# Kernel tuning notes

Hardware: AMD Instinct MI355X
Metric: run time of the kernel (lower is better)

Reference implementation:

```python
import jax, jax.numpy as jnp
import numpy as np

B, L, D = 2, 2048, 1024
H, NL = 16, 8
DH = D // H  # 64


def setup_inputs() -> dict:
    key = jax.random.key(0)
    ks = jax.random.split(key, 16)
    s_d = 1.0 / np.sqrt(D)
    s_ff = 1.0 / np.sqrt(4 * D)
    f32 = jnp.float32
    return {
        "x": jax.random.normal(ks[0], (B, L, D), f32),
        "pe": jax.random.normal(ks[1], (L, D), f32) / 10.0,
        "wq": jax.random.normal(ks[2], (NL, D, D), f32) * s_d,
        "wk": jax.random.normal(ks[3], (NL, D, D), f32) * s_d,
        "wv": jax.random.normal(ks[4], (NL, D, D), f32) * s_d,
        "ln1_g": 1.0 + 0.02 * jax.random.normal(ks[5], (NL, D), f32),
        "ln1_b": 0.02 * jax.random.normal(ks[6], (NL, D), f32),
        "w1": jax.random.normal(ks[7], (NL, D, 4 * D), f32) * s_d,
        "b1": jax.random.normal(ks[8], (NL, 4 * D), f32) * s_d,
        "w2": jax.random.normal(ks[9], (NL, 4 * D, D), f32) * s_ff,
        "b2": jax.random.normal(ks[10], (NL, D), f32) * s_ff,
        "ln2_g": 1.0 + 0.02 * jax.random.normal(ks[11], (NL, D), f32),
        "ln2_b": 0.02 * jax.random.normal(ks[12], (NL, D), f32),
    }


def _layernorm(x, g, b, eps=1e-5):
    m = jnp.mean(x, axis=-1, keepdims=True)
    v = jnp.mean(jnp.square(x - m), axis=-1, keepdims=True)
    return (x - m) * jax.lax.rsqrt(v + eps) * g + b


def reference(x, pe, wq, wk, wv, ln1_g, ln1_b, w1, b1, w2, b2, ln2_g, ln2_b):
    Bb, T, Dd = x.shape
    h = x + pe[:T]
    causal = jnp.tril(jnp.ones((T, T), dtype=bool))  # [T,T]
    inv_sqrt_dh = np.float32(1.0 / np.sqrt(DH))

    def step(h, p):
        wq_, wk_, wv_, g1, be1, w1_, bb1, w2_, bb2, g2, be2 = p
        # QKV: [B,T,D] -> [B,H,T,DH]
        q = (h @ wq_).reshape(Bb, T, H, DH).transpose(0, 2, 1, 3)
        k = (h @ wk_).reshape(Bb, T, H, DH).transpose(0, 2, 1, 3)
        v = (h @ wv_).reshape(Bb, T, H, DH).transpose(0, 2, 1, 3)
        scores = jnp.einsum('bhqd,bhkd->bhqk', q, k)
        scores = jnp.where(causal, scores, -jnp.inf)
        attn = jax.nn.softmax(scores * inv_sqrt_dh, axis=-1)
        o = jnp.einsum('bhqk,bhkd->bhqd', attn, v)
        o = o.transpose(0, 2, 1, 3).reshape(Bb, T, Dd)
        h = _layernorm(h + o, g1, be1)
        mlp = jax.nn.selu(h @ w1_ + bb1) @ w2_ + bb2
        h = _layernorm(h + mlp, g2, be2)
        return h, None

    h, _ = jax.lax.scan(step, h, (wq, wk, wv, ln1_g, ln1_b, w1, b1, w2, b2, ln2_g, ln2_b))
    return h
```

## Files before the change

kernel.cpp:

```cpp
#include <hip/hip_runtime.h>
#include <stdint.h>

typedef unsigned short u16;
typedef __bf16 bf16x8 __attribute__((ext_vector_type(8)));
typedef __bf16 bf16x4 __attribute__((ext_vector_type(4)));
typedef float f32x4 __attribute__((ext_vector_type(4)));

__device__ __forceinline__ float b2f(u16 b) {
    return __builtin_bit_cast(float, ((unsigned)b) << 16);
}
__device__ __forceinline__ u16 f2b(float f) {
    unsigned u = __builtin_bit_cast(unsigned, f);
    return (u16)((u + 0x7fffu + ((u >> 16) & 1u)) >> 16);
}
__device__ __forceinline__ void async16(const void* g, void* l) {
    __builtin_amdgcn_global_load_lds((const __attribute__((address_space(1))) void*)g,
                                     (__attribute__((address_space(3))) void*)l, 16, 0, 0);
}

__global__ __launch_bounds__(256) void add_pe_kernel(const float* __restrict__ x,
                                                     const float* __restrict__ pe,
                                                     float* __restrict__ hf,
                                                     u16* __restrict__ hb) {
    const size_t i = ((size_t)blockIdx.x * 256 + threadIdx.x) * 4;
    float4 xv = *(const float4*)(x + i);
    float4 pv = *(const float4*)(pe + (i & 2097151));
    float4 f;
    f.x = xv.x + pv.x; f.y = xv.y + pv.y; f.z = xv.z + pv.z; f.w = xv.w + pv.w;
    *(float4*)(hf + i) = f;
    ushort4 hv;
    hv.x = f2b(f.x); hv.y = f2b(f.y); hv.z = f2b(f.z); hv.w = f2b(f.w);
    *(ushort4*)(hb + i) = hv;
}

__global__ __launch_bounds__(256) void transpose_cast_kernel(const float* __restrict__ src0,
                                                             u16* __restrict__ dst0,
                                                             int srcStride, int K,
                                                             int srcLayer, int dstLayer) {
    __shared__ __align__(16) u16 tile[64 * 72];
    const float* src = src0 + (size_t)blockIdx.z * srcLayer;
    u16* dst = dst0 + (size_t)blockIdx.z * dstLayer;
    const int n0 = blockIdx.x * 64, k0 = blockIdx.y * 64;
    const int t = threadIdx.x;
    const int r = t >> 3, c8 = (t & 7) * 8;
#pragma unroll
    for (int ph = 0; ph < 2; ph++) {
        const int rr = r + ph * 32;
        const float* s = src + (size_t)(k0 + rr) * srcStride + n0 + c8;
        float4 a = *(const float4*)s;
        float4 b = *(const float4*)(s + 4);
        u16* tr = tile + rr * 72 + c8;
        tr[0] = f2b(a.x); tr[1] = f2b(a.y); tr[2] = f2b(a.z); tr[3] = f2b(a.w);
        tr[4] = f2b(b.x); tr[5] = f2b(b.y); tr[6] = f2b(b.z); tr[7] = f2b(b.w);
    }
    __syncthreads();
#pragma unroll
    for (int ph = 0; ph < 2; ph++) {
        const int rr = r + ph * 32;
        union { float4 f; u16 u[8]; } ov;
#pragma unroll
        for (int j = 0; j < 8; j++) ov.u[j] = tile[(c8 + j) * 72 + rr];
        *(float4*)(dst + (size_t)(n0 + rr) * K + k0 + c8) = ov.f;
    }
}

__global__ __launch_bounds__(256) void transpose_qkv_kernel(const float* __restrict__ wq,
                                                            const float* __restrict__ wk,
                                                            const float* __restrict__ wv,
                                                            u16* __restrict__ dst) {
    __shared__ __align__(16) u16 tile[64 * 72];
    const int zz = blockIdx.z;
    const int l = zz / 3, mat = zz - l * 3;
    const float* src = ((mat == 0) ? wq : (mat == 1) ? wk : wv) + (size_t)l * 1048576;
    u16* d = dst + (size_t)l * 3145728 + (size_t)mat * 1048576;
    const int n0 = blockIdx.x * 64, k0 = blockIdx.y * 64;
    const int t = threadIdx.x;
    const int r = t >> 3, c8 = (t & 7) * 8;
#pragma unroll
    for (int ph = 0; ph < 2; ph++) {
        const int rr = r + ph * 32;
        const float* s = src + (size_t)(k0 + rr) * 1024 + n0 + c8;
        float4 a = *(const float4*)s;
        float4 b = *(const float4*)(s + 4);
        u16* tr = tile + rr * 72 + c8;
        tr[0] = f2b(a.x); tr[1] = f2b(a.y); tr[2] = f2b(a.z); tr[3] = f2b(a.w);
        tr[4] = f2b(b.x); tr[5] = f2b(b.y); tr[6] = f2b(b.z); tr[7] = f2b(b.w);
    }
    __syncthreads();
#pragma unroll
    for (int ph = 0; ph < 2; ph++) {
        const int rr = r + ph * 32;
        union { float4 f; u16 u[8]; } ov;
#pragma unroll
        for (int j = 0; j < 8; j++) ov.u[j] = tile[(c8 + j) * 72 + rr];
        *(float4*)(d + (size_t)(n0 + rr) * 1024 + k0 + c8) = ov.f;
    }
}

__global__ __launch_bounds__(256) void transpose_v_kernel(const u16* __restrict__ src,
                                                          u16* __restrict__ dst) {
    __shared__ __align__(16) u16 tile[64 * 72];
    const int bh = blockIdx.y, t0 = blockIdx.x * 64;
    const int t = threadIdx.x;
    const int r = t >> 3, c8 = (t & 7) * 8;
    const size_t base = (size_t)bh * 131072;
#pragma unroll
    for (int ph = 0; ph < 2; ph++) {
        const int rr = r + ph * 32;
        *(float4*)(tile + rr * 72 + c8) = *(const float4*)(src + base + (size_t)(t0 + rr) * 64 + c8);
    }
    __syncthreads();
#pragma unroll
    for (int ph = 0; ph < 2; ph++) {
        const int rr = r + ph * 32;
        union { float4 f; u16 u[8]; } ov;
#pragma unroll
        for (int j = 0; j < 8; j++) ov.u[j] = tile[(c8 + j) * 72 + rr];
        *(float4*)(dst + base + (size_t)rr * 2048 + t0 + c8) = ov.f;
    }
}

#define G_SYNC1()                                          \
    __builtin_amdgcn_sched_barrier(0);                     \
    __builtin_amdgcn_s_barrier();                          \
    asm volatile("s_waitcnt lgkmcnt(0)" ::: "memory");     \
    __builtin_amdgcn_sched_barrier(0);                     \
    __builtin_amdgcn_s_setprio(1)
#define G_SYNC2()                                          \
    __builtin_amdgcn_s_setprio(0);                         \
    __builtin_amdgcn_sched_barrier(0);                     \
    __builtin_amdgcn_s_barrier()

template <int MODE, int NT>
__global__ __launch_bounds__(512) void gemm256_kernel(const u16* __restrict__ A,
                                                      const u16* __restrict__ BT,
                                                      const float* __restrict__ bias,
                                                      void* __restrict__ O0, void* __restrict__ O1,
                                                      void* __restrict__ O2, int N, int Kstride) {
    __shared__ __align__(16) u16 lds[65536];
    const int tid = threadIdx.x;
    const int lane = tid & 63, w = tid >> 6, quad = lane >> 4, l15 = lane & 15;
    const int wm = w >> 2, wn = w & 3;
    const int m0 = blockIdx.y * 256, n0 = blockIdx.x * 256;
    const size_t koff = (size_t)blockIdx.z * (NT * 64);

    f32x4 acc[8][4] = {};

    const int srow = tid >> 2;
    const int slog = (tid & 3) ^ ((tid >> 3) & 3);
    const u16* pA = A + (size_t)(m0 + srow) * Kstride + koff + slog * 8;
    const u16* pB = BT + (size_t)(n0 + srow) * Kstride + koff + slog * 8;
    u16* const ldst = lds + tid * 8;

    const int swz = (quad ^ ((l15 >> 1) & 3)) * 8;
    const int aro = (wm * 128 + l15) * 32 + swz;
    const int bro = 16384 + (wn * 64 + l15) * 32 + swz;

    auto stA = [&](int tt, int kh) {
        u16* d = ldst + ((tt & 1) << 15) + (kh << 13);
        const u16* s = pA + tt * 64 + kh * 32;
        async16(s, d);
        async16(s + (size_t)128 * Kstride, d + 4096);
    };
    auto stB = [&](int tt, int kh) {
        u16* d = ldst + ((tt & 1) << 15) + 16384 + (kh << 13);
        const u16* s = pB + tt * 64 + kh * 32;
        async16(s, d);
        async16(s + (size_t)128 * Kstride, d + 4096);
    };

    stB(0, 0); stB(0, 1); stA(0, 0); stA(0, 1);
    stB(1, 0); stB(1, 1); stA(1, 0);
    asm volatile("s_waitcnt vmcnt(6)" ::: "memory");
    __builtin_amdgcn_s_barrier();

#pragma unroll 2
    for (int t = 0; t < NT; ++t) {
        const int boff = (t & 1) << 15;
        bf16x8 a[4], bk0[4], bk1[4];
#pragma unroll
        for (int i = 0; i < 4; i++) a[i] = *(const bf16x8*)(lds + boff + aro + i * 512);
#pragma unroll
        for (int i = 0; i < 4; i++) bk0[i] = *(const bf16x8*)(lds + boff + bro + i * 512);
        if (t + 1 < NT) stA(t + 1, 1);
        G_SYNC1();
#pragma unroll
        for (int mt = 0; mt < 4; mt++)
#pragma unroll
            for (int nt = 0; nt < 4; nt++)
                acc[mt][nt] = __builtin_amdgcn_mfma_f32_16x16x32_bf16(a[mt], bk0[nt], acc[mt][nt], 0, 0, 0);
        G_SYNC2();
#pragma unroll
        for (int i = 0; i < 4; i++) a[i] = *(const bf16x8*)(lds + boff + 8192 + aro + i * 512);
#pragma unroll
        for (int i = 0; i < 4; i++) bk1[i] = *(const bf16x8*)(lds + boff + 8192 + bro + i * 512);
        if (t + 2 < NT) stB(t + 2, 0);
        G_SYNC1();
#pragma unroll
        for (int mt = 0; mt < 4; mt++)
#pragma unroll
            for (int nt = 0; nt < 4; nt++)
                acc[mt][nt] = __builtin_amdgcn_mfma_f32_16x16x32_bf16(a[mt], bk1[nt], acc[mt][nt], 0, 0, 0);
        G_SYNC2();
#pragma unroll
        for (int i = 0; i < 4; i++) a[i] = *(const bf16x8*)(lds + boff + aro + 2048 + i * 512);
        if (t + 2 < NT) stB(t + 2, 1);
        G_SYNC1();
#pragma unroll
        for (int mt = 0; mt < 4; mt++)
#pragma unroll
            for (int nt = 0; nt < 4; nt++)
                acc[4 + mt][nt] = __builtin_amdgcn_mfma_f32_16x16x32_bf16(a[mt], bk0[nt], acc[4 + mt][nt], 0, 0, 0);
        G_SYNC2();
#pragma unroll
        for (int i = 0; i < 4; i++) a[i] = *(const bf16x8*)(lds + boff + 8192 + aro + 2048 + i * 512);
        if (t + 2 < NT) stA(t + 2, 0);
        G_SYNC1();
#pragma unroll
        for (int mt = 0; mt < 4; mt++)
#pragma unroll
            for (int nt = 0; nt < 4; nt++)
                acc[4 + mt][nt] = __builtin_amdgcn_mfma_f32_16x16x32_bf16(a[mt], bk1[nt], acc[4 + mt][nt], 0, 0, 0);
        __builtin_amdgcn_s_setprio(0);
        __builtin_amdgcn_sched_barrier(0);
        if (t < NT - 2) {
            asm volatile("s_waitcnt vmcnt(6)" ::: "memory");
        } else if (t == NT - 2) {
            asm volatile("s_waitcnt vmcnt(0)" ::: "memory");
        }
        __builtin_amdgcn_sched_barrier(0);
        __builtin_amdgcn_s_barrier();
    }

#pragma unroll
    for (int nt = 0; nt < 4; nt++) {
        const int col = n0 + wn * 64 + nt * 16 + l15;
        float bv = 0.f;
        if (MODE == 1) bv = bias[col];
#pragma unroll
        for (int am = 0; am < 8; am++) {
#pragma unroll
            for (int r = 0; r < 4; r++) {
                const int row = m0 + wm * 128 + am * 16 + quad * 4 + r;
                float val = acc[am][nt][r];
                if (MODE == 0) {
                    const int mat = col >> 10, cc = col & 1023;
                    const int head = cc >> 6, dh = cc & 63;
                    const int b = row >> 11, tt = row & 2047;
                    if (mat == 0) val *= 0.18033688f;
                    u16* dst = (mat == 0) ? (u16*)O0 : (mat == 1) ? (u16*)O1 : (u16*)O2;
                    dst[(((size_t)(b * 16 + head)) * 2048 + tt) * 64 + dh] = f2b(val);
                } else if (MODE == 1) {
                    val += bv;
                    const float s = 1.0507009873554805f, aa = 1.6732632423543772f;
                    val = val > 0.f ? s * val : s * aa * (__expf(val) - 1.f);
                    ((u16*)O0)[(size_t)row * N + col] = f2b(val);
                } else if (MODE == 4) {
                    ((float*)O0)[((size_t)blockIdx.z * 4096 + row) * N + col] = val;
                }
            }
        }
    }
}

__global__ __launch_bounds__(256) void attn_kernel(const u16* __restrict__ q,
                                                   const u16* __restrict__ k,
                                                   const u16* __restrict__ vT,
                                                   u16* __restrict__ o) {
    __shared__ __align__(16) u16 Kt[2][4096];
    __shared__ __align__(16) u16 Vt[2][4096];
    __shared__ __align__(16) u16 Pt[4][32 * 72];
    const int tid = threadIdx.x, lane = tid & 63, w = tid >> 6, quad = lane >> 4, l15 = lane & 15;
    const int bh = blockIdx.x;
    const int qt = 15 - blockIdx.y;
    const size_t base = (size_t)bh * 131072;
    const int wrow0 = qt * 128 + w * 32;

    const int r0 = tid >> 3, s0 = (tid & 7) ^ (r0 & 7);
    const int r1 = (tid + 256) >> 3, s1 = (tid & 7) ^ (r1 & 7);
    const u16* kg0 = k + base + r0 * 64 + s0 * 8;
    const u16* kg1 = k + base + r1 * 64 + s1 * 8;
    const u16* vg0 = vT + base + (size_t)r0 * 2048 + s0 * 8;
    const u16* vg1 = vT + base + (size_t)r1 * 2048 + s1 * 8;

    auto stage = [&](int kt, int b) {
        async16(kg0 + kt * 4096, &Kt[b][tid * 8]);
        async16(kg1 + kt * 4096, &Kt[b][tid * 8 + 2048]);
        async16(vg0 + (size_t)kt * 64, &Vt[b][tid * 8]);
        async16(vg1 + (size_t)kt * 64, &Vt[b][tid * 8 + 2048]);
    };

    const int sA = (quad ^ (l15 & 7)) * 8;
    const int sB = sA ^ 32;

    bf16x8 qf[2][2];
#pragma unroll
    for (int nt = 0; nt < 2; nt++)
#pragma unroll
        for (int ks = 0; ks < 2; ks++)
            qf[nt][ks] = *(const bf16x8*)(q + base + (size_t)(wrow0 + nt * 16 + l15) * 64 + ks * 32 + quad * 8);

    float m_[2], l_[2];
    m_[0] = m_[1] = -1e30f;
    l_[0] = l_[1] = 0.f;
    f32x4 oacc[2][4] = {};

    const int ktmax = (qt + 1) * 2;
    stage(0, 0);

    for (int kt = 0; kt < ktmax; kt++) {
        const int cur = kt & 1;
        if (kt + 1 < ktmax) {
            stage(kt + 1, cur ^ 1);
            __builtin_amdgcn_sched_barrier(0);
            asm volatile("s_waitcnt vmcnt(4)" ::: "memory");
        } else {
            __builtin_amdgcn_sched_barrier(0);
            asm volatile("s_waitcnt vmcnt(0)" ::: "memory");
        }
        __builtin_amdgcn_sched_barrier(0);
        __builtin_amdgcn_s_barrier();
        __builtin_amdgcn_sched_barrier(0);
        const u16* Kb = Kt[cur];
        const u16* Vb = Vt[cur];
        const bool act = (kt * 64 <= wrow0 + 31);
        if (act) {
            f32x4 st[4][2];
            __builtin_amdgcn_s_setprio(1);
#pragma unroll
            for (int mt = 0; mt < 4; mt++) {
                bf16x8 kf0 = *(const bf16x8*)(Kb + (mt * 16 + l15) * 64 + sA);
                bf16x8 kf1 = *(const bf16x8*)(Kb + (mt * 16 + l15) * 64 + sB);
#pragma unroll
                for (int nt = 0; nt < 2; nt++) {
                    f32x4 z = {};
                    z = __builtin_amdgcn_mfma_f32_16x16x32_bf16(kf0, qf[nt][0], z, 0, 0, 0);
                    z = __builtin_amdgcn_mfma_f32_16x16x32_bf16(kf1, qf[nt][1], z, 0, 0, 0);
                    st[mt][nt] = z;
                }
            }
            __builtin_amdgcn_s_setprio(0);
            const bool needmask = (kt * 64 + 63 > wrow0);
            float alpha[2];
#pragma unroll
            for (int nt = 0; nt < 2; nt++) {
                const int qg = wrow0 + nt * 16 + l15;
                float mx = -1e30f;
                if (needmask) {
#pragma unroll
                    for (int mt = 0; mt < 4; mt++)
#pragma unroll
                        for (int r = 0; r < 4; r++) {
                            const int kg = kt * 64 + mt * 16 + quad * 4 + r;
                            float s = (kg <= qg) ? st[mt][nt][r] : -1e30f;
                            st[mt][nt][r] = s;
                            mx = fmaxf(mx, s);
                        }
                } else {
#pragma unroll
                    for (int mt = 0; mt < 4; mt++)
#pragma unroll
                        for (int r = 0; r < 4; r++) mx = fmaxf(mx, st[mt][nt][r]);
                }
                mx = fmaxf(mx, __shfl_xor(mx, 16, 64));
                mx = fmaxf(mx, __shfl_xor(mx, 32, 64));
                const float mnew = fmaxf(m_[nt], mx);
                alpha[nt] = exp2f(m_[nt] - mnew);
                m_[nt] = mnew;
                float rs = 0.f;
#pragma unroll
                for (int mt = 0; mt < 4; mt++) {
                    float p0 = exp2f(st[mt][nt][0] - mnew);
                    float p1 = exp2f(st[mt][nt][1] - mnew);
                    float p2 = exp2f(st[mt][nt][2] - mnew);
                    float p3 = exp2f(st[mt][nt][3] - mnew);
                    rs += (p0 + p1) + (p2 + p3);
                    bf16x4 pk = {(__bf16)p0, (__bf16)p1, (__bf16)p2, (__bf16)p3};
                    *(bf16x4*)(Pt[w] + (nt * 16 + l15) * 72 + mt * 16 + quad * 4) = pk;
                }
                rs += __shfl_xor(rs, 16, 64);
                rs += __shfl_xor(rs, 32, 64);
                l_[nt] = l_[nt] * alpha[nt] + rs;
            }
            float arow[2][4];
#pragma unroll
            for (int mto = 0; mto < 2; mto++)
#pragma unroll
                for (int r = 0; r < 4; r++)
                    arow[mto][r] = __shfl(alpha[mto], quad * 4 + r, 64);
#pragma unroll
            for (int mto = 0; mto < 2; mto++)
#pragma unroll
                for (int ntv = 0; ntv < 4; ntv++)
#pragma unroll
                    for (int r = 0; r < 4; r++) oacc[mto][ntv][r] *= arow[mto][r];

            bf16x8 pf[2][2];
#pragma unroll
            for (int mto = 0; mto < 2; mto++)
#pragma unroll
                for (int ks = 0; ks < 2; ks++)
                    pf[mto][ks] = *(const bf16x8*)(Pt[w] + (mto * 16 + l15) * 72 + ks * 32 + quad * 8);
            __builtin_amdgcn_s_setprio(1);
#pragma unroll
            for (int ntv = 0; ntv < 4; ntv++) {
                bf16x8 vf0 = *(const bf16x8*)(Vb + (ntv * 16 + l15) * 64 + sA);
                bf16x8 vf1 = *(const bf16x8*)(Vb + (ntv * 16 + l15) * 64 + sB);
#pragma unroll
                for (int mto = 0; mto < 2; mto++) {
                    oacc[mto][ntv] = __builtin_amdgcn_mfma_f32_16x16x32_bf16(pf[mto][0], vf0, oacc[mto][ntv], 0, 0, 0);
                    oacc[mto][ntv] = __builtin_amdgcn_mfma_f32_16x16x32_bf16(pf[mto][1], vf1, oacc[mto][ntv], 0, 0, 0);
                }
            }
            __builtin_amdgcn_s_setprio(0);
        }
        __builtin_amdgcn_sched_barrier(0);
        __builtin_amdgcn_s_barrier();
        __builtin_amdgcn_sched_barrier(0);
    }

    float linv[2] = {1.f / l_[0], 1.f / l_[1]};
    float rinv[2][4];
#pragma unroll
    for (int mto = 0; mto < 2; mto++)
#pragma unroll
        for (int r = 0; r < 4; r++)
            rinv[mto][r] = __shfl(linv[mto], quad * 4 + r, 64);

    const int b = bh >> 4, hh = bh & 15;
#pragma unroll
    for (int mto = 0; mto < 2; mto++)
#pragma unroll
        for (int ntv = 0; ntv < 4; ntv++)
#pragma unroll
            for (int r = 0; r < 4; r++) {
                const int trow = wrow0 + mto * 16 + quad * 4 + r;
                const int col = hh * 64 + ntv * 16 + l15;
                o[((size_t)b * 2048 + trow) * 1024 + col] = f2b(oacc[mto][ntv][r] * rinv[mto][r]);
            }
}

template <int AM>
__global__ __launch_bounds__(256) void ln_kernel(const float* __restrict__ hin,
                                                 const void* __restrict__ addp,
                                                 const float* __restrict__ g,
                                                 const float* __restrict__ bt,
                                                 const float* __restrict__ bias2,
                                                 float* __restrict__ hf_out,
                                                 u16* __restrict__ hb_out) {
    const int w = threadIdx.x >> 6, lane = threadIdx.x & 63;
    const size_t row = (size_t)blockIdx.x * 4 + w;
    const float4* hr = (const float4*)(hin + row * 1024);
    float4 xv[4];
    float s = 0.f, s2 = 0.f;
#pragma unroll
    for (int j = 0; j < 4; j++) {
        const int idx = lane + 64 * j;
        float4 a = hr[idx];
        float4 b;
        if (AM == 1) {
            ushort4 av = ((const ushort4*)addp)[row * 256 + idx];
            b.x = b2f(av.x); b.y = b2f(av.y); b.z = b2f(av.z); b.w = b2f(av.w);
        } else {
            const float4* pp = (const float4*)addp;
            const size_t po = row * 256 + idx;
            float4 p0 = pp[po];
            float4 p1 = pp[po + 1048576];
            float4 p2 = pp[po + 2097152];
            float4 p3 = pp[po + 3145728];
            float4 bb2 = ((const float4*)bias2)[idx];
            b.x = (p0.x + p1.x) + (p2.x + p3.x) + bb2.x;
            b.y = (p0.y + p1.y) + (p2.y + p3.y) + bb2.y;
            b.z = (p0.z + p1.z) + (p2.z + p3.z) + bb2.z;
            b.w = (p0.w + p1.w) + (p2.w + p3.w) + bb2.w;
        }
        float4 x;
        x.x = a.x + b.x; x.y = a.y + b.y; x.z = a.z + b.z; x.w = a.w + b.w;
        xv[j] = x;
        s += x.x + x.y + x.z + x.w;
        s2 += x.x * x.x + x.y * x.y + x.z * x.z + x.w * x.w;
    }
#pragma unroll
    for (int mm = 1; mm < 64; mm <<= 1) { s += __shfl_xor(s, mm, 64); s2 += __shfl_xor(s2, mm, 64); }
    const float mean = s * (1.f / 1024.f);
    const float var = s2 * (1.f / 1024.f) - mean * mean;
    const float rstd = rsqrtf(var + 1e-5f);
    float4* of = (float4*)(hf_out + row * 1024);
    ushort4* ob = (ushort4*)(hb_out + row * 1024);
    const float4* gv = (const float4*)g;
    const float4* bv = (const float4*)bt;
#pragma unroll
    for (int j = 0; j < 4; j++) {
        const int idx = lane + 64 * j;
        float4 gg = gv[idx], bb = bv[idx];
        float4 x = xv[j], y;
        y.x = (x.x - mean) * rstd * gg.x + bb.x;
        y.y = (x.y - mean) * rstd * gg.y + bb.y;
        y.z = (x.z - mean) * rstd * gg.z + bb.z;
        y.w = (x.w - mean) * rstd * gg.w + bb.w;
        of[idx] = y;
        ushort4 oo;
        oo.x = f2b(y.x); oo.y = f2b(y.y); oo.z = f2b(y.z); oo.w = f2b(y.w);
        ob[idx] = oo;
    }
}

extern "C" void kernel_launch(void* const* d_in, const int* in_sizes, int n_in,
                              void* d_out, int out_size, void* d_ws, size_t ws_size,
                              hipStream_t stream) {
    const float* x   = (const float*)d_in[0];
    const float* pe  = (const float*)d_in[1];
    const float* wq  = (const float*)d_in[2];
    const float* wk  = (const float*)d_in[3];
    const float* wv  = (const float*)d_in[4];
    const float* l1g = (const float*)d_in[5];
    const float* l1b = (const float*)d_in[6];
    const float* w1  = (const float*)d_in[7];
    const float* b1  = (const float*)d_in[8];
    const float* w2  = (const float*)d_in[9];
    const float* b2  = (const float*)d_in[10];
    const float* l2g = (const float*)d_in[11];
    const float* l2b = (const float*)d_in[12];

    char* ws = (char*)d_ws;
    float* hf   = (float*)(ws);
    u16* hb     = (u16*)(ws + 16777216);
    u16* qb     = (u16*)(ws + 25165824);
    u16* kb     = (u16*)(ws + 33554432);
    u16* vb     = (u16*)(ws + 41943040);
    u16* ob     = (u16*)(ws + 41943040);
    u16* vbt    = (u16*)(ws + 50331648);
    u16* ub     = (u16*)(ws + 58720256);
    float* mb   = (float*)(ws + 92274688);
    u16* wqkvT  = (u16*)(ws + 159383552);
    u16* w1T    = (u16*)(ws + 209715200);
    u16* w2T    = (u16*)(ws + 276824064);

    add_pe_kernel<<<4096, 256, 0, stream>>>(x, pe, hf, hb);
    transpose_qkv_kernel<<<dim3(16, 16, 24), 256, 0, stream>>>(wq, wk, wv, wqkvT);
    transpose_cast_kernel<<<dim3(64, 16, 8), 256, 0, stream>>>(w1, w1T, 4096, 1024, 4194304, 4194304);
    transpose_cast_kernel<<<dim3(16, 64, 8), 256, 0, stream>>>(w2, w2T, 1024, 4096, 4194304, 4194304);

    for (int l = 0; l < 8; l++) {
        gemm256_kernel<0, 16><<<dim3(12, 16), 512, 0, stream>>>(
            hb, wqkvT + (size_t)l * 3145728, nullptr, qb, kb, vb, 3072, 1024);
        transpose_v_kernel<<<dim3(32, 32), 256, 0, stream>>>(vb, vbt);
        attn_kernel<<<dim3(32, 16), 256, 0, stream>>>(qb, kb, vbt, ob);
        ln_kernel<1><<<1024, 256, 0, stream>>>(hf, ob, l1g + l * 1024, l1b + l * 1024, nullptr, hf, hb);
        gemm256_kernel<1, 16><<<dim3(16, 16), 512, 0, stream>>>(
            hb, w1T + (size_t)l * 4194304, b1 + l * 4096, ub, nullptr, nullptr, 4096, 1024);
        gemm256_kernel<4, 16><<<dim3(4, 16, 4), 512, 0, stream>>>(
            ub, w2T + (size_t)l * 4194304, nullptr, mb, nullptr, nullptr, 1024, 4096);
        const bool last = (l == 7);
        ln_kernel<2><<<1024, 256, 0, stream>>>(hf, mb, l2g + l * 1024, l2b + l * 1024,
                                               b2 + l * 1024, last ? (float*)d_out : hf, hb);
    }
}
```

Before: 2.190 ms.

## Shrink attention blocks to 64 query rows and add lazy softmax rescaling

```diff
diff --git a/kernel.cpp b/kernel.cpp
--- a/kernel.cpp
+++ b/kernel.cpp
@@ -263,35 +263,37 @@
     }
 }
 
-__global__ __launch_bounds__(256) void attn_kernel(const u16* __restrict__ q,
+__global__ __launch_bounds__(128) void attn_kernel(const u16* __restrict__ q,
                                                    const u16* __restrict__ k,
                                                    const u16* __restrict__ vT,
                                                    u16* __restrict__ o) {
     __shared__ __align__(16) u16 Kt[2][4096];
     __shared__ __align__(16) u16 Vt[2][4096];
-    __shared__ __align__(16) u16 Pt[4][32 * 72];
+    __shared__ __align__(16) u16 Pt[2][2048];
     const int tid = threadIdx.x, lane = tid & 63, w = tid >> 6, quad = lane >> 4, l15 = lane & 15;
     const int bh = blockIdx.x;
-    const int qt = 15 - blockIdx.y;
+    const int qb = 31 - blockIdx.y;
     const size_t base = (size_t)bh * 131072;
-    const int wrow0 = qt * 128 + w * 32;
-
-    const int r0 = tid >> 3, s0 = (tid & 7) ^ (r0 & 7);
-    const int r1 = (tid + 256) >> 3, s1 = (tid & 7) ^ (r1 & 7);
-    const u16* kg0 = k + base + r0 * 64 + s0 * 8;
-    const u16* kg1 = k + base + r1 * 64 + s1 * 8;
-    const u16* vg0 = vT + base + (size_t)r0 * 2048 + s0 * 8;
-    const u16* vg1 = vT + base + (size_t)r1 * 2048 + s1 * 8;
+    const int wrow0 = qb * 64 + w * 32;
+    const int ktmax = qb + 1;
+
+    const int sr = tid >> 3;
+    const int ss = (tid & 7) ^ (sr & 7);
+    const u16* kg = k + base + sr * 64 + ss * 8;
+    const u16* vg = vT + base + (size_t)sr * 2048 + ss * 8;
 
     auto stage = [&](int kt, int b) {
-        async16(kg0 + kt * 4096, &Kt[b][tid * 8]);
-        async16(kg1 + kt * 4096, &Kt[b][tid * 8 + 2048]);
-        async16(vg0 + (size_t)kt * 64, &Vt[b][tid * 8]);
-        async16(vg1 + (size_t)kt * 64, &Vt[b][tid * 8 + 2048]);
+#pragma unroll
+        for (int i = 0; i < 4; i++)
+            async16(kg + kt * 4096 + i * 1024, &Kt[b][tid * 8 + i * 1024]);
+#pragma unroll
+        for (int i = 0; i < 4; i++)
+            async16(vg + kt * 64 + i * 32768, &Vt[b][tid * 8 + i * 1024]);
     };
 
     const int sA = (quad ^ (l15 & 7)) * 8;
     const int sB = sA ^ 32;
+    const int lx = l15 & 7, qh = quad >> 1, qlow = quad & 1;
 
     bf16x8 qf[2][2];
 #pragma unroll
@@ -305,7 +307,6 @@
     l_[0] = l_[1] = 0.f;
     f32x4 oacc[2][4] = {};
 
-    const int ktmax = (qt + 1) * 2;
     stage(0, 0);
 
     for (int kt = 0; kt < ktmax; kt++) {
@@ -313,7 +314,7 @@
         if (kt + 1 < ktmax) {
             stage(kt + 1, cur ^ 1);
             __builtin_amdgcn_sched_barrier(0);
-            asm volatile("s_waitcnt vmcnt(4)" ::: "memory");
+            asm volatile("s_waitcnt vmcnt(8)" ::: "memory");
         } else {
             __builtin_amdgcn_sched_barrier(0);
             asm volatile("s_waitcnt vmcnt(0)" ::: "memory");
@@ -323,8 +324,7 @@
         __builtin_amdgcn_sched_barrier(0);
         const u16* Kb = Kt[cur];
         const u16* Vb = Vt[cur];
-        const bool act = (kt * 64 <= wrow0 + 31);
-        if (act) {
+        {
             f32x4 st[4][2];
             __builtin_amdgcn_s_setprio(1);
 #pragma unroll
@@ -340,8 +340,9 @@
                 }
             }
             __builtin_amdgcn_s_setprio(0);
-            const bool needmask = (kt * 64 + 63 > wrow0);
+            const bool needmask = (kt == qb);
             float alpha[2];
+            int needresc = 0;
 #pragma unroll
             for (int nt = 0; nt < 2; nt++) {
                 const int qg = wrow0 + nt * 16 + l15;
@@ -351,8 +352,8 @@
                     for (int mt = 0; mt < 4; mt++)
 #pragma unroll
                         for (int r = 0; r < 4; r++) {
-                            const int kg = kt * 64 + mt * 16 + quad * 4 + r;
-                            float s = (kg <= qg) ? st[mt][nt][r] : -1e30f;
+                            const int kg2 = kt * 64 + mt * 16 + quad * 4 + r;
+                            float s = (kg2 <= qg) ? st[mt][nt][r] : -1e30f;
                             st[mt][nt][r] = s;
                             mx = fmaxf(mx, s);
                         }
@@ -364,9 +365,11 @@
                 }
                 mx = fmaxf(mx, __shfl_xor(mx, 16, 64));
                 mx = fmaxf(mx, __shfl_xor(mx, 32, 64));
-                const float mnew = fmaxf(m_[nt], mx);
-                alpha[nt] = exp2f(m_[nt] - mnew);
+                const float mold = m_[nt];
+                const float mnew = (mx > mold + 8.f) ? mx : mold;
+                alpha[nt] = exp2f(mold - mnew);
                 m_[nt] = mnew;
+                needresc |= (mnew != mold) ? 1 : 0;
                 float rs = 0.f;
 #pragma unroll
                 for (int mt = 0; mt < 4; mt++) {
@@ -376,31 +379,33 @@
                     float p3 = exp2f(st[mt][nt][3] - mnew);
                     rs += (p0 + p1) + (p2 + p3);
                     bf16x4 pk = {(__bf16)p0, (__bf16)p1, (__bf16)p2, (__bf16)p3};
-                    *(bf16x4*)(Pt[w] + (nt * 16 + l15) * 72 + mt * 16 + quad * 4) = pk;
+                    *(bf16x4*)(Pt[w] + (nt * 16 + l15) * 64 + 8 * ((2 * mt + qh) ^ lx) + 4 * qlow) = pk;
                 }
                 rs += __shfl_xor(rs, 16, 64);
                 rs += __shfl_xor(rs, 32, 64);
                 l_[nt] = l_[nt] * alpha[nt] + rs;
             }
-            float arow[2][4];
+            if (__any(needresc)) {
+                float arow[2][4];
+#pragma unroll
+                for (int mto = 0; mto < 2; mto++)
+#pragma unroll
+                    for (int r = 0; r < 4; r++)
+                        arow[mto][r] = __shfl(alpha[mto], quad * 4 + r, 64);
+#pragma unroll
+                for (int mto = 0; mto < 2; mto++)
+#pragma unroll
+                    for (int ntv = 0; ntv < 4; ntv++)
+#pragma unroll
+                        for (int r = 0; r < 4; r++) oacc[mto][ntv][r] *= arow[mto][r];
+            }
+
+            bf16x8 pf[2][2];
 #pragma unroll
             for (int mto = 0; mto < 2; mto++)
 #pragma unroll
-                for (int r = 0; r < 4; r++)
-                    arow[mto][r] = __shfl(alpha[mto], quad * 4 + r, 64);
-#pragma unroll
-            for (int mto = 0; mto < 2; mto++)
-#pragma unroll
-                for (int ntv = 0; ntv < 4; ntv++)
-#pragma unroll
-                    for (int r = 0; r < 4; r++) oacc[mto][ntv][r] *= arow[mto][r];
-
-            bf16x8 pf[2][2];
-#pragma unroll
-            for (int mto = 0; mto < 2; mto++)
-#pragma unroll
                 for (int ks = 0; ks < 2; ks++)
-                    pf[mto][ks] = *(const bf16x8*)(Pt[w] + (mto * 16 + l15) * 72 + ks * 32 + quad * 8);
+                    pf[mto][ks] = *(const bf16x8*)(Pt[w] + (mto * 16 + l15) * 64 + 8 * ((4 * ks + quad) ^ lx));
             __builtin_amdgcn_s_setprio(1);
 #pragma unroll
             for (int ntv = 0; ntv < 4; ntv++) {
@@ -545,7 +550,7 @@
         gemm256_kernel<0, 16><<<dim3(12, 16), 512, 0, stream>>>(
             hb, wqkvT + (size_t)l * 3145728, nullptr, qb, kb, vb, 3072, 1024);
         transpose_v_kernel<<<dim3(32, 32), 256, 0, stream>>>(vb, vbt);
-        attn_kernel<<<dim3(32, 16), 256, 0, stream>>>(qb, kb, vbt, ob);
+        attn_kernel<<<dim3(32, 32), 128, 0, stream>>>(qb, kb, vbt, ob);
         ln_kernel<1><<<1024, 256, 0, stream>>>(hf, ob, l1g + l * 1024, l1b + l * 1024, nullptr, hf, hb);
         gemm256_kernel<1, 16><<<dim3(16, 16), 512, 0, stream>>>(
             hb, w1T + (size_t)l * 4194304, b1 + l * 4096, ub, nullptr, nullptr, 4096, 1024);
```

Result: faster. 2.105 ms (-3.9%).
